# Performance work log

Hardware: AMD Instinct MI355X
Metric: run time of the kernel (lower is better)

Reference implementation:

```python
import jax, jax.numpy as jnp
import numpy as np

LN_EPS = 1e-5


def _layernorm(x, gamma, beta):
    mu = jnp.mean(x, axis=-1, keepdims=True)
    var = jnp.mean(jnp.square(x - mu), axis=-1, keepdims=True)
    return (x - mu) * jax.lax.rsqrt(var + LN_EPS) * gamma + beta


def setup_inputs() -> dict:
    key = jax.random.key(0)
    ks = jax.random.split(key, 8)
    N, E, D = 50000, 800000, 128
    x = jax.random.normal(ks[0], (N, D), dtype=jnp.float32)
    edge_index = jax.random.randint(ks[1], (2, E), 0, N, dtype=jnp.int64)
    edge_weight = jax.random.uniform(ks[2], (E,), dtype=jnp.float32)
    dst_scale = jax.random.uniform(ks[3], (N,), dtype=jnp.float32)
    # learned params: LayerNorm affine + Linear(dim, dim)
    gamma = jnp.ones((D,), dtype=jnp.float32)
    beta = jnp.zeros((D,), dtype=jnp.float32)
    bound = float(np.sqrt(6.0 / (D + D)))  # xavier_uniform
    W = jax.random.uniform(ks[4], (D, D), minval=-bound, maxval=bound, dtype=jnp.float32)
    b = jnp.zeros((D,), dtype=jnp.float32)
    return {"x": x, "gamma": gamma, "beta": beta, "W": W, "b": b,
            "edge_index": edge_index, "num_nodes": N,
            "edge_weight": edge_weight, "dst_scale": dst_scale}


def reference(x, gamma, beta, W, b, edge_index, num_nodes, edge_weight, dst_scale):
    N = int(num_nodes)
    h = _layernorm(x, gamma, beta)            # [N, D]
    m = h @ W.T + b                           # [N, D]
    src = edge_index[0]
    dst = edge_index[1]
    w = edge_weight.astype(jnp.float32)
    msg = m[src] * w[:, None].astype(m.dtype)  # [E, D] gather + weight
    out = jax.ops.segment_sum(msg, dst, num_segments=N)       # scatter-add
    deg = jax.ops.segment_sum(w, dst, num_segments=N)         # weighted degree
    out = out / jnp.maximum(deg, 1.0)[:, None]
    out = out * dst_scale.astype(out.dtype)[:, None]
    y = x + jax.nn.gelu(out, approximate=False)  # dropout=0 -> identity
    return y
```

## Files before the change

kernel.cpp:

```cpp
#include <hip/hip_runtime.h>
#include <hip/hip_bf16.h>
#include <math.h>

typedef __attribute__((ext_vector_type(8))) short short8v;
typedef __attribute__((ext_vector_type(4))) float f32x4;

#define NBUK_CAP 2048
#define BSH      5
#define BDST     32
#define CAP      1024
#define CH       6656
#define PUNROLL  26

__global__ __launch_bounds__(256) void prep_kernel(
    const float* __restrict__ W, __hip_bfloat16* __restrict__ Wb,
    int* __restrict__ bcnt, int nbuk)
{
    const int i = blockIdx.x * 256 + threadIdx.x;
    Wb[i] = __float2bfloat16(W[i]);
    if (i < nbuk) bcnt[i] = 0;
}

__global__ __launch_bounds__(256) void count_kernel(
    const int* __restrict__ ei, int* __restrict__ bcnt, int E, int nbuk)
{
    __shared__ int h[NBUK_CAP];
    for (int j = threadIdx.x; j < nbuk; j += 256) h[j] = 0;
    __syncthreads();
    for (int e = blockIdx.x * 256 + threadIdx.x; e < E; e += gridDim.x * 256)
        atomicAdd(&h[ei[E + e] >> BSH], 1);
    __syncthreads();
    for (int j = threadIdx.x; j < nbuk; j += 256)
        if (h[j]) atomicAdd(&bcnt[j], h[j]);
}

__global__ __launch_bounds__(256) void bscan_kernel(
    const int* __restrict__ bcnt, int* __restrict__ base,
    int* __restrict__ cursor, int nbuk, int E)
{
    __shared__ int wsum[4];
    const int t = threadIdx.x;
    const int lane = t & 63;
    const int wave = t >> 6;
    int v[8];
    int s = 0;
    #pragma unroll
    for (int k = 0; k < 8; ++k) {
        const int i = t * 8 + k;
        v[k] = (i < nbuk) ? bcnt[i] : 0;
        s += v[k];
    }
    int incl = s;
    #pragma unroll
    for (int off = 1; off < 64; off <<= 1) {
        int u = __shfl_up(incl, off);
        if (lane >= off) incl += u;
    }
    if (lane == 63) wsum[wave] = incl;
    __syncthreads();
    int wpre = 0;
    #pragma unroll
    for (int w = 0; w < 4; ++w) if (w < wave) wpre += wsum[w];
    int e = wpre + incl - s;
    #pragma unroll
    for (int k = 0; k < 8; ++k) {
        const int i = t * 8 + k;
        if (i < nbuk) { base[i] = e; cursor[i] = e; }
        e += v[k];
    }
    if (t == 0) base[nbuk] = E;
}

__global__ __launch_bounds__(256) void fused_gemm_part_kernel(
    const float* __restrict__ x, const float* __restrict__ gamma,
    const float* __restrict__ beta, const __hip_bfloat16* __restrict__ Wb,
    const float* __restrict__ bias, __hip_bfloat16* __restrict__ m, int N,
    const int* __restrict__ ei, const float* __restrict__ ew,
    int* __restrict__ cursor, uint2* __restrict__ tmp, int E, int nGemm,
    int nbuk)
{
    __shared__ char smem[16384];
    const int tid = threadIdx.x;

    if ((int)blockIdx.x >= nGemm) {
        int* ph = (int*)smem;
        int* pb = ph + NBUK_CAP;
        const int e0 = (blockIdx.x - nGemm) * CH;
        for (int j = tid; j < nbuk; j += 256) ph[j] = 0;
        __syncthreads();
        int rnk[PUNROLL], dst[PUNROLL];
        #pragma unroll
        for (int i = 0; i < PUNROLL; ++i) {
            const int e = e0 + i * 256 + tid;
            rnk[i] = 0; dst[i] = -1;
            if (e < E) {
                dst[i] = ei[E + e];
                rnk[i] = atomicAdd(&ph[dst[i] >> BSH], 1);
            }
        }
        __syncthreads();
        for (int j = tid; j < nbuk; j += 256)
            pb[j] = ph[j] ? atomicAdd(&cursor[j], ph[j]) : 0;
        __syncthreads();
        #pragma unroll
        for (int i = 0; i < PUNROLL; ++i) {
            const int e = e0 + i * 256 + tid;
            if (e < E) {
                const int d = dst[i];
                const int pos = pb[d >> BSH] + rnk[i];
                uint2 kv;
                kv.x = (uint)ei[e] | ((uint)(d & (BDST - 1)) << 16);
                kv.y = __float_as_uint(ew[e]);
                tmp[pos] = kv;
            }
        }
        return;
    }

    const int lane = tid & 63;
    const int wave = tid >> 6;
    const int row0 = blockIdx.x * 64 + wave * 16;
    char* sliceb = smem + wave * 4096;

    const float2 g  = *(const float2*)&gamma[2 * lane];
    const float2 be = *(const float2*)&beta[2 * lane];

    for (int r = 0; r < 16; ++r) {
        const int row = row0 + r;
        float2 v = make_float2(0.0f, 0.0f);
        if (row < N) v = *(const float2*)&x[(size_t)row * 128 + 2 * lane];
        float s = v.x + v.y;
        #pragma unroll
        for (int off = 32; off; off >>= 1) s += __shfl_xor(s, off);
        const float mu = s * 0.0078125f;
        const float d0 = v.x - mu, d1 = v.y - mu;
        float q = d0 * d0 + d1 * d1;
        #pragma unroll
        for (int off = 32; off; off >>= 1) q += __shfl_xor(q, off);
        const float rstd = rsqrtf(q * 0.0078125f + 1e-5f);
        const float h0 = d0 * rstd * g.x + be.x;
        const float h1 = d1 * rstd * g.y + be.y;
        uint packed = (uint)__bfloat16_as_ushort(__float2bfloat16(h0))
                    | ((uint)__bfloat16_as_ushort(__float2bfloat16(h1)) << 16);
        *(uint*)(sliceb + r * 256 + ((lane * 4) ^ ((r & 7) << 4))) = packed;
    }

    const int halfsel = lane >> 4;
    const int jrow    = lane & 15;
    f32x4 acc[8];
    #pragma unroll
    for (int t = 0; t < 8; ++t)
        acc[t] = *(const f32x4*)&bias[t * 16 + halfsel * 4];

    #pragma unroll
    for (int kk = 0; kk < 4; ++kk) {
        const int boff = jrow * 256 + ((kk * 64 + halfsel * 16) ^ ((jrow & 7) << 4));
        short8v hfrag = *(const short8v*)(sliceb + boff);
        #pragma unroll
        for (int t = 0; t < 8; ++t) {
            short8v wfrag = *(const short8v*)&Wb[(size_t)(t * 16 + jrow) * 128
                                                 + kk * 32 + halfsel * 8];
            acc[t] = __builtin_amdgcn_mfma_f32_16x16x32_bf16(wfrag, hfrag, acc[t], 0, 0, 0);
        }
    }

    const int orow = row0 + jrow;
    if (orow < N) {
        #pragma unroll
        for (int t = 0; t < 8; ++t) {
            uint2 o;
            o.x = (uint)__bfloat16_as_ushort(__float2bfloat16(acc[t][0]))
                | ((uint)__bfloat16_as_ushort(__float2bfloat16(acc[t][1])) << 16);
            o.y = (uint)__bfloat16_as_ushort(__float2bfloat16(acc[t][2]))
                | ((uint)__bfloat16_as_ushort(__float2bfloat16(acc[t][3])) << 16);
            *(uint2*)&m[(size_t)orow * 128 + t * 16 + halfsel * 4] = o;
        }
    }
}

__device__ __forceinline__ float gelu_exact(float t) {
    return 0.5f * t * (1.0f + erff(t * 0.70710678118654752f));
}
__device__ __forceinline__ float bf_lo(uint p) {
    return __uint_as_float((p & 0xffffu) << 16);
}
__device__ __forceinline__ float bf_hi(uint p) {
    return __uint_as_float(p & 0xffff0000u);
}

__global__ __launch_bounds__(256) void sortgather_kernel(
    const __hip_bfloat16* __restrict__ m, const int* __restrict__ base,
    const uint2* __restrict__ tmp, const float* __restrict__ x,
    const float* __restrict__ dsc, float* __restrict__ y, int N)
{
    __shared__ uint2 led[CAP];
    __shared__ int hist[BDST], offs[BDST], cur[BDST];
    const int tid = threadIdx.x;
    const int lo  = blockIdx.x << BSH;
    const int s0  = base[blockIdx.x];
    const int cnt = base[blockIdx.x + 1] - s0;

    if (tid < BDST) { hist[tid] = 0; cur[tid] = 0; }
    __syncthreads();
    for (int i = tid; i < cnt; i += 256)
        atomicAdd(&hist[(tmp[s0 + i].x >> 16) & (BDST - 1)], 1);
    __syncthreads();
    if (tid < BDST) {
        const int v = hist[tid];
        int incl = v;
        #pragma unroll
        for (int off = 1; off < BDST; off <<= 1) {
            int u = __shfl_up(incl, off);
            if (tid >= off) incl += u;
        }
        offs[tid] = incl - v;
    }
    __syncthreads();
    for (int i = tid; i < cnt; i += 256) {
        const uint2 kv = tmp[s0 + i];
        const int dl = (kv.x >> 16) & (BDST - 1);
        const int p = offs[dl] + atomicAdd(&cur[dl], 1);
        if (p < CAP) led[p] = kv;
    }
    __syncthreads();

    const int lane = tid & 63;
    const int wv = tid >> 6;
    const uint* mu = (const uint*)m;
    for (int q = 0; q < 8; ++q) {
        const int dl = wv * 8 + q;
        const int d = lo + dl;
        if (d >= N) break;
        const int sA = offs[dl];
        const int eA = min(sA + hist[dl], CAP);
        float ax = 0.0f, ay = 0.0f, deg = 0.0f;
        int j = sA;
        for (; j + 8 <= eA; j += 8) {
            uint pv[8];
            float wj[8];
            #pragma unroll
            for (int k = 0; k < 8; ++k) {
                const uint2 kv = led[j + k];
                wj[k] = __uint_as_float(kv.y);
                pv[k] = mu[(size_t)(kv.x & 0xffff) * 64 + lane];
            }
            #pragma unroll
            for (int k = 0; k < 8; ++k) {
                ax = fmaf(wj[k], bf_lo(pv[k]), ax);
                ay = fmaf(wj[k], bf_hi(pv[k]), ay);
                deg += wj[k];
            }
        }
        for (; j < eA; ++j) {
            const uint2 kv = led[j];
            const float wl = __uint_as_float(kv.y);
            const uint pv = mu[(size_t)(kv.x & 0xffff) * 64 + lane];
            ax = fmaf(wl, bf_lo(pv), ax);
            ay = fmaf(wl, bf_hi(pv), ay);
            deg += wl;
        }
        const float sc = dsc[d] / fmaxf(deg, 1.0f);
        const float2 xv = *(const float2*)&x[(size_t)d * 128 + 2 * lane];
        float2 r;
        r.x = xv.x + gelu_exact(ax * sc);
        r.y = xv.y + gelu_exact(ay * sc);
        *(float2*)&y[(size_t)d * 128 + 2 * lane] = r;
    }
}

extern "C" void kernel_launch(void* const* d_in, const int* in_sizes, int n_in,
                              void* d_out, int out_size, void* d_ws, size_t ws_size,
                              hipStream_t stream) {
    const float* x     = (const float*)d_in[0];
    const float* gamma = (const float*)d_in[1];
    const float* beta  = (const float*)d_in[2];
    const float* W     = (const float*)d_in[3];
    const float* bias  = (const float*)d_in[4];
    const int*   ei    = (const int*)d_in[5];
    const float* ew    = (const float*)d_in[7];
    const float* dsc   = (const float*)d_in[8];

    const int N = in_sizes[0] / 128;
    const int E = in_sizes[5] / 2;
    const int nbuk = (N + BDST - 1) / BDST;

    float* y = (float*)d_out;

    __hip_bfloat16* m  = (__hip_bfloat16*)d_ws;
    __hip_bfloat16* Wb = m + (size_t)N * 128;
    int*   bcnt   = (int*)(Wb + 16384);
    int*   base   = bcnt + NBUK_CAP;
    int*   cursor = base + NBUK_CAP + 1;
    uint2* tmp    = (uint2*)(cursor + NBUK_CAP);

    prep_kernel<<<64, 256, 0, stream>>>(W, Wb, bcnt, nbuk);
    count_kernel<<<256, 256, 0, stream>>>(ei, bcnt, E, nbuk);
    bscan_kernel<<<1, 256, 0, stream>>>(bcnt, base, cursor, nbuk, E);

    const int nGemm = (N + 63) / 64;
    const int nPart = (E + CH - 1) / CH;
    fused_gemm_part_kernel<<<nGemm + nPart, 256, 0, stream>>>(
        x, gamma, beta, Wb, bias, m, N, ei, ew, cursor, tmp, E, nGemm, nbuk);

    sortgather_kernel<<<nbuk, 256, 0, stream>>>(m, base, tmp, x, dsc, y, N);
}
```

Measured before the change: 177.0 us.

## Fold weight conversion into count kernel, reorder partition blocks first, vectorize layernorm

Removes the separate prep kernel by converting W to bf16 inside count_kernel and zeroing bucket counts with hipMemsetAsync; the count grid shrinks to 192 blocks. The fused kernel now places the partition blocks before the GEMM blocks so the longer scatter work is scheduled first. Layernorm reads float4 per lane, processes two rows per wave iteration, and computes the variance in a single pass as E[x^2]-mu^2 with interleaved reductions. The single-pass variance is slightly less numerically robust, and the memset is still a separate launch on the stream.

```diff
diff --git a/kernel.cpp b/kernel.cpp
--- a/kernel.cpp
+++ b/kernel.cpp
@@ -12,22 +12,16 @@
 #define CH       6656
 #define PUNROLL  26
 
-__global__ __launch_bounds__(256) void prep_kernel(
-    const float* __restrict__ W, __hip_bfloat16* __restrict__ Wb,
-    int* __restrict__ bcnt, int nbuk)
-{
-    const int i = blockIdx.x * 256 + threadIdx.x;
-    Wb[i] = __float2bfloat16(W[i]);
-    if (i < nbuk) bcnt[i] = 0;
-}
-
 __global__ __launch_bounds__(256) void count_kernel(
-    const int* __restrict__ ei, int* __restrict__ bcnt, int E, int nbuk)
+    const int* __restrict__ ei, int* __restrict__ bcnt, int E, int nbuk,
+    const float* __restrict__ W, __hip_bfloat16* __restrict__ Wb)
 {
     __shared__ int h[NBUK_CAP];
+    const int gi = blockIdx.x * 256 + threadIdx.x;
+    if (gi < 16384) Wb[gi] = __float2bfloat16(W[gi]);
     for (int j = threadIdx.x; j < nbuk; j += 256) h[j] = 0;
     __syncthreads();
-    for (int e = blockIdx.x * 256 + threadIdx.x; e < E; e += gridDim.x * 256)
+    for (int e = gi; e < E; e += gridDim.x * 256)
         atomicAdd(&h[ei[E + e] >> BSH], 1);
     __syncthreads();
     for (int j = threadIdx.x; j < nbuk; j += 256)
@@ -71,21 +65,21 @@
     if (t == 0) base[nbuk] = E;
 }
 
-__global__ __launch_bounds__(256) void fused_gemm_part_kernel(
+__global__ __launch_bounds__(256) void fused_part_gemm_kernel(
     const float* __restrict__ x, const float* __restrict__ gamma,
     const float* __restrict__ beta, const __hip_bfloat16* __restrict__ Wb,
     const float* __restrict__ bias, __hip_bfloat16* __restrict__ m, int N,
     const int* __restrict__ ei, const float* __restrict__ ew,
-    int* __restrict__ cursor, uint2* __restrict__ tmp, int E, int nGemm,
+    int* __restrict__ cursor, uint2* __restrict__ tmp, int E, int nPart,
     int nbuk)
 {
     __shared__ char smem[16384];
     const int tid = threadIdx.x;
 
-    if ((int)blockIdx.x >= nGemm) {
+    if ((int)blockIdx.x < nPart) {
         int* ph = (int*)smem;
         int* pb = ph + NBUK_CAP;
-        const int e0 = (blockIdx.x - nGemm) * CH;
+        const int e0 = blockIdx.x * CH;
         for (int j = tid; j < nbuk; j += 256) ph[j] = 0;
         __syncthreads();
         int rnk[PUNROLL], dst[PUNROLL];
@@ -119,30 +113,40 @@
 
     const int lane = tid & 63;
     const int wave = tid >> 6;
-    const int row0 = blockIdx.x * 64 + wave * 16;
+    const int row0 = (blockIdx.x - nPart) * 64 + wave * 16;
     char* sliceb = smem + wave * 4096;
 
-    const float2 g  = *(const float2*)&gamma[2 * lane];
-    const float2 be = *(const float2*)&beta[2 * lane];
-
-    for (int r = 0; r < 16; ++r) {
+    const int c  = lane & 31;
+    const int rh = lane >> 5;
+    const float4 g4 = *(const float4*)&gamma[c * 4];
+    const float4 b4 = *(const float4*)&beta[c * 4];
+
+    #pragma unroll
+    for (int rr = 0; rr < 8; ++rr) {
+        const int r = rr * 2 + rh;
         const int row = row0 + r;
-        float2 v = make_float2(0.0f, 0.0f);
-        if (row < N) v = *(const float2*)&x[(size_t)row * 128 + 2 * lane];
-        float s = v.x + v.y;
-        #pragma unroll
-        for (int off = 32; off; off >>= 1) s += __shfl_xor(s, off);
-        const float mu = s * 0.0078125f;
-        const float d0 = v.x - mu, d1 = v.y - mu;
-        float q = d0 * d0 + d1 * d1;
-        #pragma unroll
-        for (int off = 32; off; off >>= 1) q += __shfl_xor(q, off);
-        const float rstd = rsqrtf(q * 0.0078125f + 1e-5f);
-        const float h0 = d0 * rstd * g.x + be.x;
-        const float h1 = d1 * rstd * g.y + be.y;
-        uint packed = (uint)__bfloat16_as_ushort(__float2bfloat16(h0))
-                    | ((uint)__bfloat16_as_ushort(__float2bfloat16(h1)) << 16);
-        *(uint*)(sliceb + r * 256 + ((lane * 4) ^ ((r & 7) << 4))) = packed;
+        float4 v = make_float4(0.0f, 0.0f, 0.0f, 0.0f);
+        if (row < N) v = *(const float4*)&x[(size_t)row * 128 + c * 4];
+        float s1 = (v.x + v.y) + (v.z + v.w);
+        float s2 = fmaf(v.x, v.x, fmaf(v.y, v.y, fmaf(v.z, v.z, v.w * v.w)));
+        #pragma unroll
+        for (int off = 1; off < 32; off <<= 1) {
+            s1 += __shfl_xor(s1, off);
+            s2 += __shfl_xor(s2, off);
+        }
+        const float mu   = s1 * 0.0078125f;
+        const float var  = fmaf(-mu, mu, s2 * 0.0078125f);
+        const float rstd = rsqrtf(var + 1e-5f);
+        const float h0 = (v.x - mu) * rstd * g4.x + b4.x;
+        const float h1 = (v.y - mu) * rstd * g4.y + b4.y;
+        const float h2 = (v.z - mu) * rstd * g4.z + b4.z;
+        const float h3 = (v.w - mu) * rstd * g4.w + b4.w;
+        uint2 pk;
+        pk.x = (uint)__bfloat16_as_ushort(__float2bfloat16(h0))
+             | ((uint)__bfloat16_as_ushort(__float2bfloat16(h1)) << 16);
+        pk.y = (uint)__bfloat16_as_ushort(__float2bfloat16(h2))
+             | ((uint)__bfloat16_as_ushort(__float2bfloat16(h3)) << 16);
+        *(uint2*)(sliceb + r * 256 + ((c * 8) ^ ((r & 7) << 4))) = pk;
     }
 
     const int halfsel = lane >> 4;
@@ -293,14 +297,14 @@
     int*   cursor = base + NBUK_CAP + 1;
     uint2* tmp    = (uint2*)(cursor + NBUK_CAP);
 
-    prep_kernel<<<64, 256, 0, stream>>>(W, Wb, bcnt, nbuk);
-    count_kernel<<<256, 256, 0, stream>>>(ei, bcnt, E, nbuk);
+    hipMemsetAsync(bcnt, 0, NBUK_CAP * sizeof(int), stream);
+    count_kernel<<<192, 256, 0, stream>>>(ei, bcnt, E, nbuk, W, Wb);
     bscan_kernel<<<1, 256, 0, stream>>>(bcnt, base, cursor, nbuk, E);
 
     const int nGemm = (N + 63) / 64;
     const int nPart = (E + CH - 1) / CH;
-    fused_gemm_part_kernel<<<nGemm + nPart, 256, 0, stream>>>(
-        x, gamma, beta, Wb, bias, m, N, ei, ew, cursor, tmp, E, nGemm, nbuk);
+    fused_part_gemm_kernel<<<nPart + nGemm, 256, 0, stream>>>(
+        x, gamma, beta, Wb, bias, m, N, ei, ew, cursor, tmp, E, nPart, nbuk);
 
     sortgather_kernel<<<nbuk, 256, 0, stream>>>(m, base, tmp, x, dsc, y, N);
 }
```

Measured after the change: 175.7 us. Within noise of the previous version (-0.7%).
